# Optimization experiments

Hardware: AMD Instinct MI355X
Metric: run time of the kernel (lower is better)

Reference implementation:

```python
import jax, jax.numpy as jnp
import numpy as np

EPS = 1e-12  # F.normalize default eps


def _unfold(x, p):
    """im2col matching nn.Unfold(kernel_size=p, padding=p//2).
    x: (B,C,H,W) -> (B, C, p*p, H*W), kernel positions ordered row-major."""
    B, C, H, W = x.shape
    pad = p // 2
    xp = jnp.pad(x, ((0, 0), (0, 0), (pad, pad), (pad, pad)))
    shifts = [xp[:, :, i:i + H, j:j + W] for i in range(p) for j in range(p)]
    patches = jnp.stack(shifts, axis=2)  # (B,C,p*p,H,W)
    return patches.reshape(B, C, p * p, H * W)


def setup_inputs() -> dict:
    key = jax.random.key(0)
    k1, k2 = jax.random.split(key)
    B, C, H, W = 4, 128, 128, 128
    fe_lv = jax.random.normal(k1, (B, C, H, W), dtype=jnp.float32)
    fused_features = jax.random.normal(k2, (B, C, H, W), dtype=jnp.float32)
    return {"fe_lv": fe_lv, "fused_features": fused_features}


def reference(fe_lv, fused_features):
    p = 3
    B, C, H, W = fe_lv.shape
    K = p * p
    patches = _unfold(fused_features, p)          # (B,C,K,HW)
    fe_flat = fe_lv.reshape(B, C, H * W)          # (B,C,HW)

    # L2 normalize over channel dim (dim=1), clamped like F.normalize
    pn = patches / jnp.maximum(jnp.linalg.norm(patches, axis=1, keepdims=True), EPS)
    fn = fe_flat / jnp.maximum(jnp.linalg.norm(fe_flat, axis=1, keepdims=True), EPS)

    # cosine similarity per pixel over the K neighbors: (B,HW,K)
    cos = jnp.einsum('bckn,bcn->bnk', pn, fn)
    weights = jax.nn.softmax(cos, axis=-1)        # (B,HW,K)

    # weighted aggregation of (unnormalized) patches: (B,C,HW)
    refined = jnp.einsum('bnk,bckn->bcn', weights, patches)
    return refined.reshape(B, C, H, W) + fe_lv
```

## Files before the change

### kernel.cpp

```cpp
#include <hip/hip_runtime.h>
#include <math.h>

#define C_DIM 128
#define H_DIM 128
#define W_DIM 128
#define HW (H_DIM * W_DIM)
#define EPS_N 1e-12f
#define NT 512
#define NW 8
#define CPW 16
#define LD2(p) (*(const float2*)(p))
#define LD4(p) (*(const float4*)(p))

__global__ __launch_bounds__(256) void norms_fu4(const float* __restrict__ fu,
                                                 float* __restrict__ rn)
{
    __shared__ float4 part[32][9];
    const int tid = threadIdx.x;
    const int li = tid & 31;
    const int g = tid >> 5;
    const float* p = fu + (size_t)blockIdx.y * C_DIM * HW + (size_t)g * 16 * HW
                     + blockIdx.x * 128 + 4 * li;
    float4 s = make_float4(0.f, 0.f, 0.f, 0.f);
#pragma unroll
    for (int j = 0; j < 16; ++j) {
        const float4 v = LD4(p + (size_t)j * HW);
        s.x += v.x * v.x; s.y += v.y * v.y;
        s.z += v.z * v.z; s.w += v.w * v.w;
    }
    part[li][g] = s;
    __syncthreads();
    if (tid < 32) {
        float4 t = make_float4(0.f, 0.f, 0.f, 0.f);
#pragma unroll
        for (int gg = 0; gg < 8; ++gg) {
            const float4 q = part[tid][gg];
            t.x += q.x; t.y += q.y; t.z += q.z; t.w += q.w;
        }
        float4 r;
        r.x = 1.f / fmaxf(sqrtf(t.x), EPS_N);
        r.y = 1.f / fmaxf(sqrtf(t.y), EPS_N);
        r.z = 1.f / fmaxf(sqrtf(t.z), EPS_N);
        r.w = 1.f / fmaxf(sqrtf(t.w), EPS_N);
        *(float4*)(rn + (size_t)blockIdx.y * HW + blockIdx.x * 128 + 4 * tid) = r;
    }
}

__global__ __launch_bounds__(NT) void asfr_main3(const float* __restrict__ fe,
                                                 const float* __restrict__ fu,
                                                 const float* __restrict__ rn,
                                                 float* __restrict__ out)
{
    __shared__ float part[NW][10][W_DIM];
    __shared__ float wl[9][W_DIM];
    __shared__ float n2r[3][W_DIM];

    const int tid = threadIdx.x;
    const int l   = tid & 63;
    const int wv  = tid >> 6;

    const int bid = blockIdx.x;
    const int cpx = gridDim.x >> 3;
    const int wb  = (bid & 7) * cpx + (bid >> 3);
    const int bz  = wb >> 7;
    const int row = wb & 127;

    const size_t imgbase = (size_t)bz * C_DIM * HW;
    const int c0   = wv * CPW;
    const int col0 = 2 * l;

    if (tid < 3 * W_DIM) {
        const int r = tid >> 7, c = tid & 127;
        const int nr = row + r - 1;
        float v = 1.f;
        if (nr >= 0 && nr < H_DIM) v = rn[(size_t)bz * HW + nr * W_DIM + c];
        n2r[r][c] = v;
    }

    const bool has_u = (row > 0), has_d = (row < H_DIM - 1);
    const int rup = has_u ? row - 1 : row;
    const int rdn = has_d ? row + 1 : row;

    const float* pfe = fe + imgbase + (size_t)c0 * HW + row * W_DIM + col0;
    const float* pfm = fu + imgbase + (size_t)c0 * HW + row * W_DIM + col0;
    const float* pfu = fu + imgbase + (size_t)c0 * HW + rup * W_DIM + col0;
    const float* pfd = fu + imgbase + (size_t)c0 * HW + rdn * W_DIM + col0;
    const float2 z2 = make_float2(0.f, 0.f);

    auto ldpair = [&](int jb, float2& f0, float2& u0, float2& m0, float2& d0,
                      float2& f1, float2& u1, float2& m1, float2& d1) {
        const size_t oA = (size_t)(2 * jb) * HW;
        const size_t oB = oA + HW;
        f0 = LD2(pfe + oA); u0 = LD2(pfu + oA); m0 = LD2(pfm + oA); d0 = LD2(pfd + oA);
        f1 = LD2(pfe + oB); u1 = LD2(pfu + oB); m1 = LD2(pfm + oB); d1 = LD2(pfd + oB);
        if (!has_u) { u0 = z2; u1 = z2; }
        if (!has_d) { d0 = z2; d1 = z2; }
    };

    float2 dk[9];
#pragma unroll
    for (int k = 0; k < 9; ++k) dk[k] = z2;
    float2 fe2 = z2;

    auto acc3 = [&](const float2 f, const float2 v, const int r3) {
        float lft = __shfl_up(v.y, 1);   lft = (l == 0)  ? 0.f : lft;
        float rgt = __shfl_down(v.x, 1); rgt = (l == 63) ? 0.f : rgt;
        dk[r3+0].x += f.x * lft;  dk[r3+1].x += f.x * v.x;  dk[r3+2].x += f.x * v.y;
        dk[r3+0].y += f.y * v.x;  dk[r3+1].y += f.y * v.y;  dk[r3+2].y += f.y * rgt;
    };

    {
        float2 fA, uA, mA, dA, fB, uB, mB, dB;
        ldpair(0, fA, uA, mA, dA, fB, uB, mB, dB);
#pragma unroll
        for (int jb = 0; jb < CPW / 2; ++jb) {
            float2 nfA, nuA, nmA, ndA, nfB, nuB, nmB, ndB;
            if (jb + 1 < CPW / 2)
                ldpair(jb + 1, nfA, nuA, nmA, ndA, nfB, nuB, nmB, ndB);
            fe2.x += fA.x * fA.x + fB.x * fB.x;
            fe2.y += fA.y * fA.y + fB.y * fB.y;
            acc3(fA, uA, 0); acc3(fA, mA, 3); acc3(fA, dA, 6);
            acc3(fB, uB, 0); acc3(fB, mB, 3); acc3(fB, dB, 6);
            if (jb + 1 < CPW / 2) {
                fA = nfA; uA = nuA; mA = nmA; dA = ndA;
                fB = nfB; uB = nuB; mB = nmB; dB = ndB;
            }
        }
    }

#pragma unroll
    for (int k = 0; k < 9; ++k) *(float2*)&part[wv][k][col0] = dk[k];
    *(float2*)&part[wv][9][col0] = fe2;

    float2 c2fA, c2uA, c2mA, c2dA, c2fB, c2uB, c2mB, c2dB;
    ldpair(0, c2fA, c2uA, c2mA, c2dA, c2fB, c2uB, c2mB, c2dB);
    __syncthreads();

    if (tid < W_DIM) {
        const int px = tid;
        float dv[10];
#pragma unroll
        for (int k = 0; k < 10; ++k) {
            float s = 0.f;
#pragma unroll
            for (int w = 0; w < NW; ++w) s += part[w][k][px];
            dv[k] = s;
        }
        const float rfe = 1.f / fmaxf(sqrtf(dv[9]), EPS_N);
        float cs[9];
        float mx = -1e30f;
#pragma unroll
        for (int k = 0; k < 9; ++k) {
            const int di = k / 3, dj = k % 3;
            const int nr = row + di - 1;
            const int nc = px + dj - 1;
            const bool ok = (nr >= 0 && nr < H_DIM && nc >= 0 && nc < W_DIM);
            const int ncc = min(max(nc, 0), W_DIM - 1);
            const float cv = ok ? dv[k] * rfe * n2r[di][ncc] : 0.f;
            cs[k] = cv;
            mx = fmaxf(mx, cv);
        }
        float sum = 0.f;
#pragma unroll
        for (int k = 0; k < 9; ++k) { cs[k] = __expf(cs[k] - mx); sum += cs[k]; }
        const float is = 1.f / sum;
#pragma unroll
        for (int k = 0; k < 9; ++k) wl[k][px] = cs[k] * is;
    }
    __syncthreads();

    float2 w2[9];
#pragma unroll
    for (int k = 0; k < 9; ++k) w2[k] = *(const float2*)&wl[k][col0];

    auto agg3 = [&](float2& acc, const float2 w9[9], const float2 v, const int r3) {
        float lft = __shfl_up(v.y, 1);   lft = (l == 0)  ? 0.f : lft;
        float rgt = __shfl_down(v.x, 1); rgt = (l == 63) ? 0.f : rgt;
        acc.x += w9[r3+0].x * lft  + w9[r3+1].x * v.x + w9[r3+2].x * v.y;
        acc.y += w9[r3+0].y * v.x  + w9[r3+1].y * v.y + w9[r3+2].y * rgt;
    };

    float* pout = out + imgbase + (size_t)c0 * HW + row * W_DIM + col0;
#pragma unroll
    for (int jb = 0; jb < CPW / 2; ++jb) {
        float2 nfA, nuA, nmA, ndA, nfB, nuB, nmB, ndB;
        if (jb + 1 < CPW / 2)
            ldpair(jb + 1, nfA, nuA, nmA, ndA, nfB, nuB, nmB, ndB);
        float2 accA = c2fA;
        float2 accB = c2fB;
        agg3(accA, w2, c2uA, 0); agg3(accA, w2, c2mA, 3); agg3(accA, w2, c2dA, 6);
        agg3(accB, w2, c2uB, 0); agg3(accB, w2, c2mB, 3); agg3(accB, w2, c2dB, 6);
        const size_t oA = (size_t)(2 * jb) * HW;
        *(float2*)(pout + oA)      = accA;
        *(float2*)(pout + oA + HW) = accB;
        if (jb + 1 < CPW / 2) {
            c2fA = nfA; c2uA = nuA; c2mA = nmA; c2dA = ndA;
            c2fB = nfB; c2uB = nuB; c2mB = nmB; c2dB = ndB;
        }
    }
}

extern "C" void kernel_launch(void* const* d_in, const int* in_sizes, int n_in,
                              void* d_out, int out_size, void* d_ws, size_t ws_size,
                              hipStream_t stream) {
    const float* fe = (const float*)d_in[0];
    const float* fu = (const float*)d_in[1];
    float* out = (float*)d_out;
    float* rn = (float*)d_ws;
    const int B = in_sizes[0] / (C_DIM * HW);

    dim3 g1(HW / 128, B);
    norms_fu4<<<g1, 256, 0, stream>>>(fu, rn);

    dim3 g2(B * H_DIM);
    asfr_main3<<<g2, NT, 0, stream>>>(fe, fu, rn, out);
}
```

Measured before the change: 41.07 us.

## Use float4 per-lane pixel layout with half-wave channel split in main kernel

```diff
diff --git a/kernel.cpp b/kernel.cpp
--- a/kernel.cpp
+++ b/kernel.cpp
@@ -9,7 +9,6 @@
 #define NT 512
 #define NW 8
 #define CPW 16
-#define LD2(p) (*(const float2*)(p))
 #define LD4(p) (*(const float4*)(p))
 
 __global__ __launch_bounds__(256) void norms_fu4(const float* __restrict__ fu,
@@ -46,7 +45,7 @@
     }
 }
 
-__global__ __launch_bounds__(NT) void asfr_main3(const float* __restrict__ fe,
+__global__ __launch_bounds__(NT) void asfr_main5(const float* __restrict__ fe,
                                                  const float* __restrict__ fu,
                                                  const float* __restrict__ rn,
                                                  float* __restrict__ out)
@@ -58,6 +57,8 @@
     const int tid = threadIdx.x;
     const int l   = tid & 63;
     const int wv  = tid >> 6;
+    const int li  = l & 31;
+    const int sub = l >> 5;
 
     const int bid = blockIdx.x;
     const int cpx = gridDim.x >> 3;
@@ -66,8 +67,8 @@
     const int row = wb & 127;
 
     const size_t imgbase = (size_t)bz * C_DIM * HW;
-    const int c0   = wv * CPW;
-    const int col0 = 2 * l;
+    const int c0  = wv * CPW;
+    const int px0 = 4 * li;
 
     if (tid < 3 * W_DIM) {
         const int r = tid >> 7, c = tid & 127;
@@ -80,60 +81,60 @@
     const bool has_u = (row > 0), has_d = (row < H_DIM - 1);
     const int rup = has_u ? row - 1 : row;
     const int rdn = has_d ? row + 1 : row;
-
-    const float* pfe = fe + imgbase + (size_t)c0 * HW + row * W_DIM + col0;
-    const float* pfm = fu + imgbase + (size_t)c0 * HW + row * W_DIM + col0;
-    const float* pfu = fu + imgbase + (size_t)c0 * HW + rup * W_DIM + col0;
-    const float* pfd = fu + imgbase + (size_t)c0 * HW + rdn * W_DIM + col0;
-    const float2 z2 = make_float2(0.f, 0.f);
-
-    auto ldpair = [&](int jb, float2& f0, float2& u0, float2& m0, float2& d0,
-                      float2& f1, float2& u1, float2& m1, float2& d1) {
-        const size_t oA = (size_t)(2 * jb) * HW;
-        const size_t oB = oA + HW;
-        f0 = LD2(pfe + oA); u0 = LD2(pfu + oA); m0 = LD2(pfm + oA); d0 = LD2(pfd + oA);
-        f1 = LD2(pfe + oB); u1 = LD2(pfu + oB); m1 = LD2(pfm + oB); d1 = LD2(pfd + oB);
-        if (!has_u) { u0 = z2; u1 = z2; }
-        if (!has_d) { d0 = z2; d1 = z2; }
-    };
-
-    float2 dk[9];
-#pragma unroll
-    for (int k = 0; k < 9; ++k) dk[k] = z2;
-    float2 fe2 = z2;
-
-    auto acc3 = [&](const float2 f, const float2 v, const int r3) {
-        float lft = __shfl_up(v.y, 1);   lft = (l == 0)  ? 0.f : lft;
-        float rgt = __shfl_down(v.x, 1); rgt = (l == 63) ? 0.f : rgt;
-        dk[r3+0].x += f.x * lft;  dk[r3+1].x += f.x * v.x;  dk[r3+2].x += f.x * v.y;
-        dk[r3+0].y += f.y * v.x;  dk[r3+1].y += f.y * v.y;  dk[r3+2].y += f.y * rgt;
-    };
-
-    {
-        float2 fA, uA, mA, dA, fB, uB, mB, dB;
-        ldpair(0, fA, uA, mA, dA, fB, uB, mB, dB);
-#pragma unroll
-        for (int jb = 0; jb < CPW / 2; ++jb) {
-            float2 nfA, nuA, nmA, ndA, nfB, nuB, nmB, ndB;
-            if (jb + 1 < CPW / 2)
-                ldpair(jb + 1, nfA, nuA, nmA, ndA, nfB, nuB, nmB, ndB);
-            fe2.x += fA.x * fA.x + fB.x * fB.x;
-            fe2.y += fA.y * fA.y + fB.y * fB.y;
-            acc3(fA, uA, 0); acc3(fA, mA, 3); acc3(fA, dA, 6);
-            acc3(fB, uB, 0); acc3(fB, mB, 3); acc3(fB, dB, 6);
-            if (jb + 1 < CPW / 2) {
-                fA = nfA; uA = nuA; mA = nmA; dA = ndA;
-                fB = nfB; uB = nuB; mB = nmB; dB = ndB;
-            }
-        }
-    }
-
-#pragma unroll
-    for (int k = 0; k < 9; ++k) *(float2*)&part[wv][k][col0] = dk[k];
-    *(float2*)&part[wv][9][col0] = fe2;
-
-    float2 c2fA, c2uA, c2mA, c2dA, c2fB, c2uB, c2mB, c2dB;
-    ldpair(0, c2fA, c2uA, c2mA, c2dA, c2fB, c2uB, c2mB, c2dB);
+    const float4 z4 = make_float4(0.f, 0.f, 0.f, 0.f);
+
+    const int offL = (li == 0) ? 0 : -1;
+    const int offR = (li == 31) ? 3 : 4;
+
+    float4 dk[9];
+#pragma unroll
+    for (int k = 0; k < 9; ++k) dk[k] = z4;
+    float4 fe24 = z4;
+
+#define TAP(P, ZR, F, R3) {                                                   \
+    float4 m_ = LD4(P);                                                       \
+    float lf_ = (P)[offL];                                                    \
+    float rf_ = (P)[offR];                                                    \
+    if (ZR) m_ = z4;                                                          \
+    if ((li == 0) || (ZR)) lf_ = 0.f;                                         \
+    if ((li == 31) || (ZR)) rf_ = 0.f;                                        \
+    dk[R3+0].x += F.x*lf_;  dk[R3+0].y += F.y*m_.x;                           \
+    dk[R3+0].z += F.z*m_.y; dk[R3+0].w += F.w*m_.z;                           \
+    dk[R3+1].x += F.x*m_.x; dk[R3+1].y += F.y*m_.y;                           \
+    dk[R3+1].z += F.z*m_.z; dk[R3+1].w += F.w*m_.w;                           \
+    dk[R3+2].x += F.x*m_.y; dk[R3+2].y += F.y*m_.z;                           \
+    dk[R3+2].z += F.z*m_.w; dk[R3+2].w += F.w*rf_; }
+
+#pragma unroll
+    for (int j = 0; j < 8; ++j) {
+        const size_t cb = imgbase + (size_t)(c0 + 2 * j + sub) * HW;
+        const float4 f = LD4(fe + cb + row * W_DIM + px0);
+        fe24.x += f.x * f.x; fe24.y += f.y * f.y;
+        fe24.z += f.z * f.z; fe24.w += f.w * f.w;
+        const float* pu = fu + cb + rup * W_DIM + px0;
+        const float* pm = fu + cb + row * W_DIM + px0;
+        const float* pd = fu + cb + rdn * W_DIM + px0;
+        TAP(pu, !has_u, f, 0)
+        TAP(pm, false,  f, 3)
+        TAP(pd, !has_d, f, 6)
+    }
+#undef TAP
+
+#pragma unroll
+    for (int k = 0; k < 9; ++k) {
+        dk[k].x += __shfl_xor(dk[k].x, 32);
+        dk[k].y += __shfl_xor(dk[k].y, 32);
+        dk[k].z += __shfl_xor(dk[k].z, 32);
+        dk[k].w += __shfl_xor(dk[k].w, 32);
+    }
+    fe24.x += __shfl_xor(fe24.x, 32); fe24.y += __shfl_xor(fe24.y, 32);
+    fe24.z += __shfl_xor(fe24.z, 32); fe24.w += __shfl_xor(fe24.w, 32);
+
+    if (sub == 0) {
+#pragma unroll
+        for (int k = 0; k < 9; ++k) *(float4*)&part[wv][k][px0] = dk[k];
+        *(float4*)&part[wv][9][px0] = fe24;
+    }
     __syncthreads();
 
     if (tid < W_DIM) {
@@ -169,35 +170,36 @@
     }
     __syncthreads();
 
-    float2 w2[9];
-#pragma unroll
-    for (int k = 0; k < 9; ++k) w2[k] = *(const float2*)&wl[k][col0];
-
-    auto agg3 = [&](float2& acc, const float2 w9[9], const float2 v, const int r3) {
-        float lft = __shfl_up(v.y, 1);   lft = (l == 0)  ? 0.f : lft;
-        float rgt = __shfl_down(v.x, 1); rgt = (l == 63) ? 0.f : rgt;
-        acc.x += w9[r3+0].x * lft  + w9[r3+1].x * v.x + w9[r3+2].x * v.y;
-        acc.y += w9[r3+0].y * v.x  + w9[r3+1].y * v.y + w9[r3+2].y * rgt;
-    };
-
-    float* pout = out + imgbase + (size_t)c0 * HW + row * W_DIM + col0;
-#pragma unroll
-    for (int jb = 0; jb < CPW / 2; ++jb) {
-        float2 nfA, nuA, nmA, ndA, nfB, nuB, nmB, ndB;
-        if (jb + 1 < CPW / 2)
-            ldpair(jb + 1, nfA, nuA, nmA, ndA, nfB, nuB, nmB, ndB);
-        float2 accA = c2fA;
-        float2 accB = c2fB;
-        agg3(accA, w2, c2uA, 0); agg3(accA, w2, c2mA, 3); agg3(accA, w2, c2dA, 6);
-        agg3(accB, w2, c2uB, 0); agg3(accB, w2, c2mB, 3); agg3(accB, w2, c2dB, 6);
-        const size_t oA = (size_t)(2 * jb) * HW;
-        *(float2*)(pout + oA)      = accA;
-        *(float2*)(pout + oA + HW) = accB;
-        if (jb + 1 < CPW / 2) {
-            c2fA = nfA; c2uA = nuA; c2mA = nmA; c2dA = ndA;
-            c2fB = nfB; c2uB = nuB; c2mB = nmB; c2dB = ndB;
-        }
-    }
+    float4 w4[9];
+#pragma unroll
+    for (int k = 0; k < 9; ++k) w4[k] = *(const float4*)&wl[k][px0];
+
+#define AGTAP(P, ZR, ACC, R3) {                                               \
+    float4 m_ = LD4(P);                                                       \
+    float lf_ = (P)[offL];                                                    \
+    float rf_ = (P)[offR];                                                    \
+    if (ZR) m_ = z4;                                                          \
+    if ((li == 0) || (ZR)) lf_ = 0.f;                                         \
+    if ((li == 31) || (ZR)) rf_ = 0.f;                                        \
+    ACC.x += w4[R3+0].x*lf_  + w4[R3+1].x*m_.x + w4[R3+2].x*m_.y;             \
+    ACC.y += w4[R3+0].y*m_.x + w4[R3+1].y*m_.y + w4[R3+2].y*m_.z;             \
+    ACC.z += w4[R3+0].z*m_.y + w4[R3+1].z*m_.z + w4[R3+2].z*m_.w;             \
+    ACC.w += w4[R3+0].w*m_.z + w4[R3+1].w*m_.w + w4[R3+2].w*rf_; }
+
+#pragma unroll
+    for (int j = 0; j < 8; ++j) {
+        const size_t cb = imgbase + (size_t)(c0 + 2 * j + sub) * HW;
+        const float4 f = LD4(fe + cb + row * W_DIM + px0);
+        const float* pu = fu + cb + rup * W_DIM + px0;
+        const float* pm = fu + cb + row * W_DIM + px0;
+        const float* pd = fu + cb + rdn * W_DIM + px0;
+        float4 acc = f;
+        AGTAP(pu, !has_u, acc, 0)
+        AGTAP(pm, false,  acc, 3)
+        AGTAP(pd, !has_d, acc, 6)
+        *(float4*)(out + cb + row * W_DIM + px0) = acc;
+    }
+#undef AGTAP
 }
 
 extern "C" void kernel_launch(void* const* d_in, const int* in_sizes, int n_in,
@@ -213,5 +215,5 @@
     norms_fu4<<<g1, 256, 0, stream>>>(fu, rn);
 
     dim3 g2(B * H_DIM);
-    asfr_main3<<<g2, NT, 0, stream>>>(fe, fu, rn, out);
+    asfr_main5<<<g2, NT, 0, stream>>>(fe, fu, rn, out);
 }
```

After: 58.29 us. +41.9%, slower.
